# Kernel optimization log

Measured on AMD Instinct MI355X. Metric: run time of the kernel, lower is better.

The kernel has to match this reference:

```python
import jax, jax.numpy as jnp
import numpy as np

NUM_HEADS = 4

def gelu(x):
    # torch nn.GELU() default is the exact (erf) form
    return jax.nn.gelu(x, approximate=False)

def setup_inputs() -> dict:
    key = jax.random.key(0)
    k0, k1, k2, k3, k4 = jax.random.split(key, 5)
    B, N, F, T = 2, 2048, 64, 12
    hidden = 32
    d = hidden // NUM_HEADS  # 8
    x = jax.random.normal(k0, (B, N, F, T), dtype=jnp.float32)
    adj = jax.random.uniform(k1, (N, N), dtype=jnp.float32)
    w1 = jax.random.normal(k2, (T,), dtype=jnp.float32) * 0.1          # W_mapping1 (out=1)
    W2 = jax.random.normal(k3, (F, hidden), dtype=jnp.float32) * 0.1   # W_mapping2
    a = jax.random.normal(k4, (2 * d + 1,), dtype=jnp.float32) * 0.1   # A_mapping (out=1)
    return {"x": x, "adj": adj, "w1": w1, "W2": W2, "a": a}

def reference(x, adj, w1, W2, a):
    H = NUM_HEADS
    B, N, F, T = x.shape
    # W_mapping1 + squeeze + GELU: (B,N,F)
    q = gelu(jnp.einsum('bnft,t->bnf', x, w1))
    # W_mapping2: (B,N,hidden)
    Q = jnp.einsum('bnf,fh->bnh', q, W2)
    hid = Q.shape[-1]
    d = hid // H
    Q4 = Q.reshape(B, N, H, d)  # per-head features
    aq, ak, aadj = a[:d], a[d:2 * d], a[2 * d]
    # A_mapping(cat(Q,K,adj)) is linear => decompose into scalar projections.
    # K[b,i,j] = Q[b,j] (permute of broadcast Q), so:
    sq = jnp.einsum('bnhd,d->bnh', Q4, aq)  # (B,N,H) query-node term
    sk = jnp.einsum('bnhd,d->bnh', Q4, ak)  # (B,N,H) key-node term
    # scores[b,i,j,h] = GELU(sq[b,i,h] + sk[b,j,h] + adj[i,j]*aadj)
    scores = gelu(sq[:, :, None, :] + sk[:, None, :, :] + adj[None, :, :, None] * aadj)
    return scores.transpose(0, 3, 1, 2)  # (B, H, N, N)
```

## Files before the change

kernel.cpp:

```cpp
#include <hip/hip_runtime.h>
#include <math.h>

#define NH 4
#define DH 8
#define NF 64
#define NT 12
#define NB 2
#define IT 4

__device__ __forceinline__ float gelu_f(float x) {
    const float s = x * 0.70710678118654752440f;
    const float z = __builtin_fabsf(s);
    const float t = __builtin_amdgcn_rcpf(fmaf(0.3275911f, z, 1.0f));
    float p = fmaf(1.061405429f, t, -1.453152027f);
    p = fmaf(p, t, 1.421413741f);
    p = fmaf(p, t, -0.284496736f);
    p = fmaf(p, t, 0.254829592f);
    p *= t;
    const float e = __builtin_amdgcn_exp2f(z * z * -1.44269504088896340736f);
    const float erfa = fmaf(-p, e, 1.0f);
    const float erfv = __builtin_copysignf(erfa, s);
    return 0.5f * x * (1.0f + erfv);
}

__global__ __launch_bounds__(256) void qk_kernel(
    const float* __restrict__ x, const float* __restrict__ w1,
    const float* __restrict__ W2, const float* __restrict__ a,
    float* __restrict__ sqT, float* __restrict__ skT, int N)
{
    __shared__ float Wq[NF][NH + 1];
    __shared__ float Wk[NF][NH + 1];
    const int t = threadIdx.x;

    {
        int f = t >> 2, h = t & 3;
        float accq = 0.f, acck = 0.f;
        #pragma unroll
        for (int k = 0; k < DH; ++k) {
            float w = W2[f * (NH * DH) + h * DH + k];
            accq += w * a[k];
            acck += w * a[DH + k];
        }
        Wq[f][h] = accq;
        Wk[f][h] = acck;
    }
    __syncthreads();

    float w1r[NT];
    #pragma unroll
    for (int i = 0; i < NT; ++i) w1r[i] = w1[i];

    const int wave = t >> 6;
    const int lane = t & 63;
    const long long row = (long long)blockIdx.x * 4 + wave;
    if (row >= (long long)NB * N) return;

    const float* xr = x + row * (NF * NT) + (long long)lane * NT;
    float4 v0 = *(const float4*)(xr);
    float4 v1 = *(const float4*)(xr + 4);
    float4 v2 = *(const float4*)(xr + 8);
    float dot = v0.x*w1r[0] + v0.y*w1r[1] + v0.z*w1r[2]  + v0.w*w1r[3]
              + v1.x*w1r[4] + v1.y*w1r[5] + v1.z*w1r[6]  + v1.w*w1r[7]
              + v2.x*w1r[8] + v2.y*w1r[9] + v2.z*w1r[10] + v2.w*w1r[11];
    float q = gelu_f(dot);

    float acc[8];
    #pragma unroll
    for (int h = 0; h < NH; ++h) {
        acc[h]     = q * Wq[lane][h];
        acc[4 + h] = q * Wk[lane][h];
    }
    #pragma unroll
    for (int ofs = 32; ofs > 0; ofs >>= 1) {
        #pragma unroll
        for (int i = 0; i < 8; ++i)
            acc[i] += __shfl_xor(acc[i], ofs, 64);
    }
    if (lane < 8) {
        int h   = lane & 3;
        int isK = lane >> 2;
        int b   = (int)(row / N);
        int n   = (int)(row % N);
        float* dst = isK ? skT : sqT;
        dst[((long long)b * NH + h) * N + n] = acc[lane];
    }
}

__global__ __launch_bounds__(256) void score_kernel_tiled(
    const float* __restrict__ adj, const float* __restrict__ sqT,
    const float* __restrict__ skT, const float* __restrict__ a,
    float* __restrict__ out, int N)
{
    const float aadj = a[2 * DH];
    const int nq  = N >> 2;
    const int wpr = nq >> 8;
    const int ig = blockIdx.x / wpr;
    const int w  = blockIdx.x - ig * wpr;
    const int i0 = ig * IT;
    const int j0 = ((w << 8) + threadIdx.x) << 2;

    float4 sk[NB * NH];
    #pragma unroll
    for (int bh = 0; bh < NB * NH; ++bh)
        sk[bh] = *(const float4*)(skT + (long long)bh * N + j0);

    #pragma unroll
    for (int ii = 0; ii < IT; ++ii) {
        const int i = i0 + ii;
        float4 adj4 = *(const float4*)(adj + (long long)i * N + j0);
        const float a0 = adj4.x * aadj;
        const float a1 = adj4.y * aadj;
        const float a2 = adj4.z * aadj;
        const float a3 = adj4.w * aadj;

        #pragma unroll
        for (int bh = 0; bh < NB * NH; ++bh) {
            const float sq = sqT[(long long)bh * N + i];
            float4 o;
            o.x = gelu_f(sq + sk[bh].x + a0);
            o.y = gelu_f(sq + sk[bh].y + a1);
            o.z = gelu_f(sq + sk[bh].z + a2);
            o.w = gelu_f(sq + sk[bh].w + a3);
            *(float4*)(out + ((long long)bh * N + i) * N + j0) = o;
        }
    }
}

__global__ __launch_bounds__(256) void score_kernel_flat(
    const float* __restrict__ adj, const float* __restrict__ sqT,
    const float* __restrict__ skT, const float* __restrict__ a,
    float* __restrict__ out, int N)
{
    const float aadj = a[2 * DH];
    const int nq = N >> 2;
    long long tid = (long long)blockIdx.x * blockDim.x + threadIdx.x;
    if (tid >= (long long)N * nq) return;
    const int i  = (int)(tid / nq);
    const int j0 = (int)(tid % nq) << 2;

    float4 adj4 = *(const float4*)(adj + (long long)i * N + j0);
    const float a0 = adj4.x * aadj;
    const float a1 = adj4.y * aadj;
    const float a2 = adj4.z * aadj;
    const float a3 = adj4.w * aadj;

    #pragma unroll
    for (int bh = 0; bh < NB * NH; ++bh) {
        const float sq = sqT[(long long)bh * N + i];
        float4 sk4 = *(const float4*)(skT + (long long)bh * N + j0);
        float4 o;
        o.x = gelu_f(sq + sk4.x + a0);
        o.y = gelu_f(sq + sk4.y + a1);
        o.z = gelu_f(sq + sk4.z + a2);
        o.w = gelu_f(sq + sk4.w + a3);
        *(float4*)(out + ((long long)bh * N + i) * N + j0) = o;
    }
}

extern "C" void kernel_launch(void* const* d_in, const int* in_sizes, int n_in,
                              void* d_out, int out_size, void* d_ws, size_t ws_size,
                              hipStream_t stream)
{
    const float* x   = (const float*)d_in[0];
    const float* adj = (const float*)d_in[1];
    const float* w1  = (const float*)d_in[2];
    const float* W2  = (const float*)d_in[3];
    const float* a   = (const float*)d_in[4];
    float* out = (float*)d_out;

    int N = 1;
    while ((long long)(N + 1) * (N + 1) <= (long long)in_sizes[1]) ++N;

    float* sqT = (float*)d_ws;
    float* skT = sqT + (size_t)NB * NH * N;

    const int rows = NB * N;
    qk_kernel<<<(rows + 3) / 4, 256, 0, stream>>>(x, w1, W2, a, sqT, skT, N);

    const int nq = N >> 2;
    if ((nq & 255) == 0 && (N % IT) == 0) {
        const int wpr = nq >> 8;
        const int blocks = (N / IT) * wpr;
        score_kernel_tiled<<<blocks, 256, 0, stream>>>(adj, sqT, skT, a, out, N);
    } else {
        const long long total = (long long)N * nq;
        score_kernel_flat<<<(int)((total + 255) / 256), 256, 0, stream>>>(adj, sqT, skT, a, out, N);
    }
}
```

Measured before the change: 34.80 us.

## Prefetch adjacency matrix into cache from extra blocks in the QK kernel

Adds extra blocks to the first kernel that read the whole adj matrix (16 MB) and discard the values. The aim is to warm the L2/last-level cache so the score kernel reads adj from cache. The QK work and the adj reads now overlap in one launch. The cost is extra blocks and memory traffic in the first kernel. The gain depends on adj staying resident in the MI355X's large last-level cache before the score kernel runs.

```diff
diff --git a/kernel.cpp b/kernel.cpp
--- a/kernel.cpp
+++ b/kernel.cpp
@@ -23,14 +23,32 @@
     return 0.5f * x * (1.0f + erfv);
 }
 
-__global__ __launch_bounds__(256) void qk_kernel(
-    const float* __restrict__ x, const float* __restrict__ w1,
-    const float* __restrict__ W2, const float* __restrict__ a,
-    float* __restrict__ sqT, float* __restrict__ skT, int N)
-{
+__global__ __launch_bounds__(256) void qk_prefetch_kernel(
+    const float* __restrict__ x, const float* __restrict__ adj,
+    const float* __restrict__ w1, const float* __restrict__ W2,
+    const float* __restrict__ a,
+    float* __restrict__ sqT, float* __restrict__ skT, int N, int qkBlocks)
+{
+    const int t = threadIdx.x;
+
+    if ((int)blockIdx.x >= qkBlocks) {
+        const int pb = (int)blockIdx.x - qkBlocks;
+        const int nq = N >> 2;
+        float keep = 0.f;
+        #pragma unroll
+        for (int r = 0; r < 2; ++r) {
+            const int i = pb * 2 + r;
+            if (i < N) {
+                const float4* arow = (const float4*)(adj + (long long)i * N);
+                for (int q = t; q < nq; q += 256) keep += arow[q].x;
+            }
+        }
+        asm volatile("" :: "v"(keep));
+        return;
+    }
+
     __shared__ float Wq[NF][NH + 1];
     __shared__ float Wk[NF][NH + 1];
-    const int t = threadIdx.x;
 
     {
         int f = t >> 2, h = t & 3;
@@ -174,8 +192,10 @@
     float* sqT = (float*)d_ws;
     float* skT = sqT + (size_t)NB * NH * N;
 
-    const int rows = NB * N;
-    qk_kernel<<<(rows + 3) / 4, 256, 0, stream>>>(x, w1, W2, a, sqT, skT, N);
+    const int qkBlocks = (NB * N + 3) / 4;
+    const int pfBlocks = (N + 1) / 2;
+    qk_prefetch_kernel<<<qkBlocks + pfBlocks, 256, 0, stream>>>(
+        x, adj, w1, W2, a, sqT, skT, N, qkBlocks);
 
     const int nq = N >> 2;
     if ((nq & 255) == 0 && (N % IT) == 0) {
```

After: 34.80 us. No clear change (+0.0%).

## Stage scaled adj tile in LDS and split batch-heads across waves

Applied to the files above, without the earlier changes.

The score kernel now loads the IT×1024 adjacency tile once into shared memory, pre-scaled by aadj. Each of the four waves then handles two of the eight (batch, head) pairs across all 1024 columns, loading its own sk values. This cuts per-thread register pressure from holding eight sk float4s and changes the work split so waves write different output planes. The cost is an LDS round trip plus a block barrier, and each thread's work per bh is now spread across four column chunks.

```diff
diff --git a/kernel.cpp b/kernel.cpp
--- a/kernel.cpp
+++ b/kernel.cpp
@@ -86,42 +86,57 @@
     }
 }
 
-__global__ __launch_bounds__(256) void score_kernel_tiled(
+__global__ __launch_bounds__(256) void score_kernel_lds(
     const float* __restrict__ adj, const float* __restrict__ sqT,
     const float* __restrict__ skT, const float* __restrict__ a,
     float* __restrict__ out, int N)
 {
     const float aadj = a[2 * DH];
+    const int t   = threadIdx.x;
     const int nq  = N >> 2;
     const int wpr = nq >> 8;
-    const int ig = blockIdx.x / wpr;
-    const int w  = blockIdx.x - ig * wpr;
-    const int i0 = ig * IT;
-    const int j0 = ((w << 8) + threadIdx.x) << 2;
-
-    float4 sk[NB * NH];
-    #pragma unroll
-    for (int bh = 0; bh < NB * NH; ++bh)
-        sk[bh] = *(const float4*)(skT + (long long)bh * N + j0);
-
-    #pragma unroll
-    for (int ii = 0; ii < IT; ++ii) {
-        const int i = i0 + ii;
-        float4 adj4 = *(const float4*)(adj + (long long)i * N + j0);
-        const float a0 = adj4.x * aadj;
-        const float a1 = adj4.y * aadj;
-        const float a2 = adj4.z * aadj;
-        const float a3 = adj4.w * aadj;
-
-        #pragma unroll
-        for (int bh = 0; bh < NB * NH; ++bh) {
-            const float sq = sqT[(long long)bh * N + i];
-            float4 o;
-            o.x = gelu_f(sq + sk[bh].x + a0);
-            o.y = gelu_f(sq + sk[bh].y + a1);
-            o.z = gelu_f(sq + sk[bh].z + a2);
-            o.w = gelu_f(sq + sk[bh].w + a3);
-            *(float4*)(out + ((long long)bh * N + i) * N + j0) = o;
+    const int ig  = blockIdx.x / wpr;
+    const int w   = blockIdx.x - ig * wpr;
+    const int i0  = ig * IT;
+    const int q0  = w << 8;
+
+    __shared__ float adjS[IT][1024];
+
+    #pragma unroll
+    for (int r = 0; r < IT; ++r) {
+        float4 v = *(const float4*)(adj + (long long)(i0 + r) * N + ((q0 + t) << 2));
+        float4 sv; sv.x = v.x * aadj; sv.y = v.y * aadj;
+                   sv.z = v.z * aadj; sv.w = v.w * aadj;
+        *(float4*)&adjS[r][t << 2] = sv;
+    }
+    __syncthreads();
+
+    const int wave = t >> 6;
+    const int lane = t & 63;
+
+    #pragma unroll
+    for (int bb = 0; bb < 2; ++bb) {
+        const int bh = (wave << 1) + bb;
+
+        float4 sk[4];
+        #pragma unroll
+        for (int k = 0; k < 4; ++k)
+            sk[k] = *(const float4*)(skT + (long long)bh * N + ((q0 + lane + (k << 6)) << 2));
+
+        #pragma unroll
+        for (int ii = 0; ii < IT; ++ii) {
+            const float sq = sqT[(long long)bh * N + i0 + ii];
+            #pragma unroll
+            for (int k = 0; k < 4; ++k) {
+                const int qw = lane + (k << 6);
+                const float* ar = &adjS[ii][qw << 2];
+                float4 o;
+                o.x = gelu_f(sq + sk[k].x + ar[0]);
+                o.y = gelu_f(sq + sk[k].y + ar[1]);
+                o.z = gelu_f(sq + sk[k].z + ar[2]);
+                o.w = gelu_f(sq + sk[k].w + ar[3]);
+                *(float4*)(out + ((long long)bh * N + i0 + ii) * N + ((q0 + qw) << 2)) = o;
+            }
         }
     }
 }
@@ -181,7 +196,7 @@
     if ((nq & 255) == 0 && (N % IT) == 0) {
         const int wpr = nq >> 8;
         const int blocks = (N / IT) * wpr;
-        score_kernel_tiled<<<blocks, 256, 0, stream>>>(adj, sqT, skT, a, out, N);
+        score_kernel_lds<<<blocks, 256, 0, stream>>>(adj, sqT, skT, a, out, N);
     } else {
         const long long total = (long long)N * nq;
         score_kernel_flat<<<(int)((total + 255) / 256), 256, 0, stream>>>(adj, sqT, skT, a, out, N);
```

After: 34.36 us, median of 2. Within noise of the previous version (-1.3%).
